# Optimization experiments

Hardware: AMD Instinct MI355X
Metric: run time of the kernel (lower is better)

## Reference

```python
import jax, jax.numpy as jnp
import numpy as np

N_NODES = 100_000
N_EDGES = 3_200_000
HIDDEN = 16


def setup_inputs() -> dict:
    key = jax.random.key(0)
    k1, k2, k3, k4 = jax.random.split(key, 4)
    x = jax.random.normal(k1, (N_NODES, 3), dtype=jnp.float32)
    edge_index = jax.random.randint(k2, (2, N_EDGES), 0, N_NODES, dtype=jnp.int32)
    # Glorot-style init for the two GCN layers (PyG GCNConv: lin weight + bias)
    W1 = jax.random.normal(k3, (3, HIDDEN), dtype=jnp.float32) * (1.0 / np.sqrt(3.0))
    b1 = jnp.zeros((HIDDEN,), dtype=jnp.float32)
    W2 = jax.random.normal(k4, (HIDDEN, 1), dtype=jnp.float32) * (1.0 / np.sqrt(HIDDEN))
    b2 = jnp.zeros((1,), dtype=jnp.float32)
    return {"x": x, "edge_index": edge_index, "W1": W1, "b1": b1, "W2": W2, "b2": b2}


def reference(x, edge_index, W1, b1, W2, b2):
    n = x.shape[0]  # static under jit
    # GCNConv default: add self-loops, symmetric degree normalization
    self_loop = jnp.arange(n, dtype=edge_index.dtype)
    src = jnp.concatenate([edge_index[0], self_loop])
    dst = jnp.concatenate([edge_index[1], self_loop])
    deg = jax.ops.segment_sum(jnp.ones_like(src, dtype=x.dtype), dst, num_segments=n)
    inv_sqrt_deg = jnp.where(deg > 0, jax.lax.rsqrt(jnp.maximum(deg, 1.0)), 0.0)
    norm = inv_sqrt_deg[src] * inv_sqrt_deg[dst]  # [E+N]

    def gcn_conv(h, W, b):
        h = h @ W  # linear transform first (cheaper: small out dim)
        msg = norm[:, None] * h[src]  # gather + scale
        return jax.ops.segment_sum(msg, dst, num_segments=n) + b  # scatter-add

    h = jax.nn.relu(gcn_conv(x, W1, b1))
    out = gcn_conv(h, W2, b2)
    return out.squeeze(-1)  # [N]
```

## Files before the change

kernel.cpp:

```cpp
#include <hip/hip_runtime.h>

#define HIDDEN 16
#define FB 128
#define FB_SHIFT 7
#define NBK_MAX 4096
#define FCHUNK 4096
#define FTH 512
#define STH 512
#define NXCD 8
#define CB 1024
#define CB_SHIFT 10
#define NCB_MAX 512
#define CHUNK 4096
#define SPL 8
#define BT 1024

__device__ __forceinline__ int xcd_chunk(int bid, int nwg) {
    if (nwg < NXCD) return bid;
    int q = nwg / NXCD, r = nwg % NXCD;
    int x = bid % NXCD, k = bid / NXCD;
    return (x < r ? x * (q + 1) : r * (q + 1) + (x - r) * q) + k;
}


__global__ __launch_bounds__(FTH) void
k_histf(const int* __restrict__ dst, int e, int nbk, int nchunk,
        unsigned int* __restrict__ hcT) {
    __shared__ unsigned int h[NBK_MAX];
    for (int i = threadIdx.x; i < nbk; i += FTH) h[i] = 0u;
    __syncthreads();
    int c = xcd_chunk(blockIdx.x, nchunk);
    int start = c * FCHUNK;
    int end = min(start + FCHUNK, e);
    if (end - start == FCHUNK) {
        int i = start + threadIdx.x;
#pragma unroll
        for (int k = 0; k < FCHUNK / FTH; k++, i += FTH)
            atomicAdd(&h[((unsigned)dst[i]) >> FB_SHIFT], 1u);
    } else {
        for (int i = start + threadIdx.x; i < end; i += FTH)
            atomicAdd(&h[((unsigned)dst[i]) >> FB_SHIFT], 1u);
    }
    __syncthreads();
    for (int j = threadIdx.x; j < nbk; j += FTH)
        hcT[(size_t)j * nchunk + c] = h[j];
}

__global__ void k_scanf(unsigned int* __restrict__ hcT,
                        unsigned int* __restrict__ cntc, int nchunk) {
    __shared__ unsigned int ts[256];
    __shared__ unsigned int carry;
    int b = blockIdx.x, t = threadIdx.x;
    if (t == 0) carry = 0u;
    __syncthreads();
    size_t row = (size_t)b * nchunk;
    for (int t0 = 0; t0 < nchunk; t0 += 256) {
        int i = t0 + t;
        unsigned int v = (i < nchunk) ? hcT[row + i] : 0u;
        ts[t] = v;
        __syncthreads();
        for (int off = 1; off < 256; off <<= 1) {
            unsigned int u = (t >= off) ? ts[t - off] : 0u;
            __syncthreads();
            ts[t] += u;
            __syncthreads();
        }
        if (i < nchunk) hcT[row + i] = carry + ts[t] - v;
        __syncthreads();
        if (t == 0) carry += ts[255];
        __syncthreads();
    }
    if (t == 0) cntc[b] = carry;
}

__global__ __launch_bounds__(1024) void
k_scanb(const unsigned int* __restrict__ cntc, int nbk,
        unsigned int* __restrict__ basec,
        unsigned int* __restrict__ rowptr, int n, unsigned int e) {
    __shared__ unsigned int tsum[1024];
    int t = threadIdx.x;
    int K = (nbk + 1023) / 1024;
    unsigned int s = 0;
    for (int k = 0; k < K; k++) {
        int i = t * K + k;
        if (i < nbk) s += cntc[i];
    }
    tsum[t] = s;
    __syncthreads();
    for (int off = 1; off < 1024; off <<= 1) {
        unsigned int v = (t >= off) ? tsum[t - off] : 0u;
        __syncthreads();
        tsum[t] += v;
        __syncthreads();
    }
    unsigned int run = (t == 0) ? 0u : tsum[t - 1];
    for (int k = 0; k < K; k++) {
        int i = t * K + k;
        if (i < nbk) { basec[i] = run; run += cntc[i]; }
    }
    if (t == 1023) basec[nbk] = tsum[1023];
    if (t == 0) rowptr[n] = e;
}

__global__ __launch_bounds__(FTH) void
k_fillf(const int* __restrict__ src, const int* __restrict__ dst,
        int e, int nbk, int nchunk,
        const unsigned int* __restrict__ basec,
        const unsigned int* __restrict__ hcT,
        unsigned int* __restrict__ tmp) {
    __shared__ unsigned int h[NBK_MAX];
    __shared__ unsigned int lb[NBK_MAX];
    int c = xcd_chunk(blockIdx.x, nchunk);
    for (int j = threadIdx.x; j < nbk; j += FTH) {
        lb[j] = basec[j] + hcT[(size_t)j * nchunk + c];
        h[j] = 0u;
    }
    __syncthreads();
    int start = c * FCHUNK;
    int end = min(start + FCHUNK, e);
    if (end - start == FCHUNK) {
        int i = start + threadIdx.x;
#pragma unroll
        for (int k = 0; k < FCHUNK / FTH; k++, i += FTH) {
            unsigned int d = (unsigned)dst[i];
            unsigned int s = (unsigned)src[i];
            unsigned int b = d >> FB_SHIFT;
            unsigned int r = atomicAdd(&h[b], 1u);
            tmp[lb[b] + r] = (s << FB_SHIFT) | (d & (FB - 1u));
        }
    } else {
        for (int i = start + threadIdx.x; i < end; i += FTH) {
            unsigned int d = (unsigned)dst[i];
            unsigned int s = (unsigned)src[i];
            unsigned int b = d >> FB_SHIFT;
            unsigned int r = atomicAdd(&h[b], 1u);
            tmp[lb[b] + r] = (s << FB_SHIFT) | (d & (FB - 1u));
        }
    }
}

__global__ __launch_bounds__(STH) void
k_sortN(const unsigned int* __restrict__ tmp,
        const unsigned int* __restrict__ basec,
        const float* __restrict__ x,
        unsigned int* __restrict__ rowptr, unsigned int* __restrict__ tmp2,
        float4* __restrict__ xs4, int n) {
    __shared__ unsigned int cnt[FB];
    __shared__ unsigned int sc[FB];
    __shared__ unsigned int cur[FB];
    int t = threadIdx.x, b = blockIdx.x;
    unsigned int s = basec[b], endp = basec[b + 1];
    if (t < FB) cnt[t] = 0u;
    __syncthreads();
    for (unsigned int i = s + t; i < endp; i += STH)
        atomicAdd(&cnt[tmp[i] & (FB - 1u)], 1u);
    __syncthreads();
    if (t < FB) sc[t] = cnt[t];
    __syncthreads();
    for (int off = 1; off < FB; off <<= 1) {
        unsigned int v = (t < FB && t >= off) ? sc[t - off] : 0u;
        __syncthreads();
        if (t < FB && t >= off) sc[t] += v;
        __syncthreads();
    }
    if (t < FB) {
        unsigned int excl = sc[t] - cnt[t];
        cur[t] = s + excl;
        int node = (b << FB_SHIFT) + t;
        if (node < n) {
            rowptr[node] = s + excl;
            float iv = rsqrtf((float)(1u + cnt[t]));
            xs4[node] = make_float4(x[3 * node] * iv, x[3 * node + 1] * iv,
                                    x[3 * node + 2] * iv, iv);
        }
    }
    __syncthreads();
    for (unsigned int i = s + t; i < endp; i += STH) {
        unsigned int rec = tmp[i];
        unsigned int r = atomicAdd(&cur[rec & (FB - 1u)], 1u);
        tmp2[r] = rec >> FB_SHIFT;
    }
}

__global__ void k_s1(const unsigned int* __restrict__ rowptr,
                     const unsigned int* __restrict__ tmp2,
                     const float4* __restrict__ xs4,
                     const float* __restrict__ W1, const float* __restrict__ b1,
                     const float* __restrict__ W2, const float* __restrict__ b2,
                     float* __restrict__ t2s, float* __restrict__ out, int n) {
    int gid = blockIdx.x * blockDim.x + threadIdx.x;
    int i = gid >> 1, h = gid & 1;
    bool valid = (i < n);
    unsigned int s = 0, epos = 0;
    if (valid) { s = rowptr[i]; epos = rowptr[i + 1]; }
    unsigned int half = (epos - s) >> 1;
    unsigned int b0 = h ? s + half : s;
    unsigned int b1r = h ? epos : s + half;
    float v0 = 0.f, v1 = 0.f, v2 = 0.f;
    unsigned int j = b0;
    for (; j + 4 <= b1r; j += 4) {
        unsigned a0 = tmp2[j], a1 = tmp2[j + 1], a2 = tmp2[j + 2], a3 = tmp2[j + 3];
        float4 p0 = xs4[a0], p1 = xs4[a1], p2 = xs4[a2], p3 = xs4[a3];
        v0 += (p0.x + p1.x) + (p2.x + p3.x);
        v1 += (p0.y + p1.y) + (p2.y + p3.y);
        v2 += (p0.z + p1.z) + (p2.z + p3.z);
    }
    for (; j < b1r; j++) {
        float4 p = xs4[tmp2[j]];
        v0 += p.x; v1 += p.y; v2 += p.z;
    }
    v0 += __shfl_xor(v0, 1);
    v1 += __shfl_xor(v1, 1);
    v2 += __shfl_xor(v2, 1);
    if (valid && h == 0) {
        float4 me = xs4[i];
        float iv = me.w;
        v0 = (v0 + me.x) * iv;
        v1 = (v1 + me.y) * iv;
        v2 = (v2 + me.z) * iv;
        float acc = 0.f;
#pragma unroll
        for (int k = 0; k < HIDDEN; k++) {
            float hh = fmaxf(fmaf(v0, W1[k], fmaf(v1, W1[HIDDEN + k],
                            fmaf(v2, W1[2 * HIDDEN + k], b1[k]))), 0.f);
            acc += hh * W2[k];
        }
        t2s[i] = acc * iv;
        out[i] = b2[0] + acc * iv * iv;
    }
}

__global__ void k_s2(const unsigned int* __restrict__ rowptr,
                     const unsigned int* __restrict__ tmp2,
                     const float* __restrict__ t2s, const float4* __restrict__ xs4,
                     float* __restrict__ out, int n) {
    int gid = blockIdx.x * blockDim.x + threadIdx.x;
    int i = gid >> 1, h = gid & 1;
    bool valid = (i < n);
    unsigned int s = 0, epos = 0;
    if (valid) { s = rowptr[i]; epos = rowptr[i + 1]; }
    unsigned int half = (epos - s) >> 1;
    unsigned int b0 = h ? s + half : s;
    unsigned int b1r = h ? epos : s + half;
    float v = 0.f;
    unsigned int j = b0;
    for (; j + 4 <= b1r; j += 4) {
        unsigned a0 = tmp2[j], a1 = tmp2[j + 1], a2 = tmp2[j + 2], a3 = tmp2[j + 3];
        v += (t2s[a0] + t2s[a1]) + (t2s[a2] + t2s[a3]);
    }
    for (; j < b1r; j++) v += t2s[tmp2[j]];
    v += __shfl_xor(v, 1);
    if (valid && h == 0) out[i] += v * xs4[i].w;
}


__global__ void k_zero(unsigned int* a, int na) {
    int i = blockIdx.x * blockDim.x + threadIdx.x;
    if (i < na) a[i] = 0u;
}
__global__ void k_hist_c(const int* __restrict__ dst, int e, int ncb, int nchunk,
                         unsigned int* __restrict__ cntc,
                         unsigned int* __restrict__ hcT) {
    __shared__ unsigned int h[NCB_MAX];
    for (int i = threadIdx.x; i < ncb; i += blockDim.x) h[i] = 0u;
    __syncthreads();
    int start = blockIdx.x * CHUNK;
    int end = min(start + CHUNK, e);
    for (int i = start + threadIdx.x; i < end; i += 256)
        atomicAdd(&h[((unsigned)dst[i]) >> CB_SHIFT], 1u);
    __syncthreads();
    for (int j = threadIdx.x; j < ncb; j += blockDim.x) {
        hcT[(size_t)j * nchunk + blockIdx.x] = h[j];
        if (h[j]) atomicAdd(&cntc[j], h[j]);
    }
}
__global__ void k_scan(const unsigned int* __restrict__ cnt, int nb,
                       unsigned int* __restrict__ base) {
    __shared__ unsigned int tsum[256];
    int t = threadIdx.x;
    int K = (nb + 255) / 256;
    unsigned int s = 0;
    for (int k = 0; k < K; k++) {
        int i = t * K + k;
        if (i < nb) s += cnt[i];
    }
    tsum[t] = s;
    __syncthreads();
    for (int off = 1; off < 256; off <<= 1) {
        unsigned int v = (t >= off) ? tsum[t - off] : 0u;
        __syncthreads();
        tsum[t] += v;
        __syncthreads();
    }
    unsigned int run = (t == 0) ? 0u : tsum[t - 1];
    for (int k = 0; k < K; k++) {
        int i = t * K + k;
        if (i < nb) { base[i] = run; run += cnt[i]; }
    }
}
__global__ void k_scanc(const unsigned int* __restrict__ hcT,
                        const unsigned int* __restrict__ basec,
                        unsigned int* __restrict__ lbasec, int nchunk) {
    __shared__ unsigned int ts[256];
    __shared__ unsigned int carry;
    int b = blockIdx.x, t = threadIdx.x;
    if (t == 0) carry = basec[b];
    __syncthreads();
    for (int t0 = 0; t0 < nchunk; t0 += 256) {
        int i = t0 + t;
        unsigned int v = (i < nchunk) ? hcT[(size_t)b * nchunk + i] : 0u;
        ts[t] = v;
        __syncthreads();
        for (int off = 1; off < 256; off <<= 1) {
            unsigned int u = (t >= off) ? ts[t - off] : 0u;
            __syncthreads();
            ts[t] += u;
            __syncthreads();
        }
        if (i < nchunk) lbasec[(size_t)b * nchunk + i] = carry + ts[t] - v;
        __syncthreads();
        if (t == 0) carry += ts[255];
        __syncthreads();
    }
}
__global__ void k_fill_c(const int* __restrict__ src, const int* __restrict__ dst,
                         int e, int ncb, int nchunk,
                         const unsigned int* __restrict__ lbasec,
                         unsigned int* __restrict__ tmp) {
    __shared__ unsigned int h[NCB_MAX];
    __shared__ unsigned int lb[NCB_MAX];
    for (int j = threadIdx.x; j < ncb; j += blockDim.x) {
        lb[j] = lbasec[(size_t)j * nchunk + blockIdx.x];
        h[j] = 0u;
    }
    __syncthreads();
    int start = blockIdx.x * CHUNK;
    int end = min(start + CHUNK, e);
    for (int i = start + threadIdx.x; i < end; i += 256) {
        unsigned int d = (unsigned)dst[i];
        unsigned int b = d >> CB_SHIFT;
        unsigned int r = atomicAdd(&h[b], 1u);
        tmp[lb[b] + r] = (((unsigned)src[i]) << CB_SHIFT) | (d & (CB - 1u));
    }
}
__global__ __launch_bounds__(BT) void
k_deg_split(const unsigned int* __restrict__ tmp, const unsigned int* __restrict__ basec,
            const unsigned int* __restrict__ cntc, unsigned int* __restrict__ deg, int n) {
    __shared__ unsigned int degl[CB];
    int t = threadIdx.x;
    degl[t] = 0u;
    __syncthreads();
    int b = blockIdx.x / SPL, sl = blockIdx.x % SPL;
    unsigned int s = basec[b], m = cntc[b];
    for (unsigned int i = sl * BT + t; i < m; i += SPL * BT)
        atomicAdd(&degl[tmp[s + i] & (CB - 1u)], 1u);
    __syncthreads();
    int node = b * CB + t;
    unsigned int c = degl[t];
    if (node < n && c) atomicAdd(&deg[node], c);
}
__global__ void k_inv_s(const unsigned int* __restrict__ deg, const float* __restrict__ x,
                        float4* __restrict__ xs4, int n) {
    int i = blockIdx.x * blockDim.x + threadIdx.x;
    if (i >= n) return;
    float iv = rsqrtf((float)(deg[i] + 1u));
    xs4[i] = make_float4(x[3 * i] * iv, x[3 * i + 1] * iv, x[3 * i + 2] * iv, iv);
}
__global__ __launch_bounds__(BT) void
k_s1_split(const unsigned int* __restrict__ tmp, const unsigned int* __restrict__ basec,
           const unsigned int* __restrict__ cntc, const float4* __restrict__ xs4,
           float* __restrict__ agg0, float* __restrict__ agg1, float* __restrict__ agg2, int n) {
    __shared__ float a0[CB], a1[CB], a2[CB];
    int t = threadIdx.x;
    a0[t] = 0.f; a1[t] = 0.f; a2[t] = 0.f;
    __syncthreads();
    int b = blockIdx.x / SPL, sl = blockIdx.x % SPL;
    unsigned int s = basec[b], m = cntc[b];
    for (unsigned int i = sl * BT + t; i < m; i += SPL * BT) {
        unsigned rec = tmp[s + i];
        float4 v = xs4[rec >> CB_SHIFT];
        unsigned dl = rec & (CB - 1u);
        atomicAdd(&a0[dl], v.x); atomicAdd(&a1[dl], v.y); atomicAdd(&a2[dl], v.z);
    }
    __syncthreads();
    int node = b * CB + t;
    if (node < n) {
        if (a0[t] != 0.f) atomicAdd(&agg0[node], a0[t]);
        if (a1[t] != 0.f) atomicAdd(&agg1[node], a1[t]);
        if (a2[t] != 0.f) atomicAdd(&agg2[node], a2[t]);
    }
}
__global__ void k_epi_s(const float* __restrict__ agg0, const float* __restrict__ agg1,
                        const float* __restrict__ agg2, const float4* __restrict__ xs4,
                        const float* __restrict__ W1, const float* __restrict__ b1,
                        const float* __restrict__ W2, const float* __restrict__ b2,
                        float* __restrict__ t2s, float* __restrict__ out, int n) {
    int i = blockIdx.x * blockDim.x + threadIdx.x;
    if (i >= n) return;
    float4 xv = xs4[i];
    float iv = xv.w;
    float v0 = iv * (agg0[i] + xv.x), v1 = iv * (agg1[i] + xv.y), v2 = iv * (agg2[i] + xv.z);
    float acc = 0.f;
#pragma unroll
    for (int j = 0; j < HIDDEN; j++) {
        float h = fmaxf(fmaf(v0, W1[j], fmaf(v1, W1[HIDDEN + j],
                       fmaf(v2, W1[2 * HIDDEN + j], b1[j]))), 0.f);
        acc += h * W2[j];
    }
    t2s[i] = acc * iv;
    out[i] = b2[0] + acc * iv * iv;
}
__global__ __launch_bounds__(BT) void
k_s2_split(const unsigned int* __restrict__ tmp, const unsigned int* __restrict__ basec,
           const unsigned int* __restrict__ cntc, const float* __restrict__ t2s,
           const float4* __restrict__ xs4, float* __restrict__ out, int n) {
    __shared__ float o[CB];
    int t = threadIdx.x;
    o[t] = 0.f;
    __syncthreads();
    int b = blockIdx.x / SPL, sl = blockIdx.x % SPL;
    unsigned int s = basec[b], m = cntc[b];
    for (unsigned int i = sl * BT + t; i < m; i += SPL * BT) {
        unsigned rec = tmp[s + i];
        atomicAdd(&o[rec & (CB - 1u)], t2s[rec >> CB_SHIFT]);
    }
    __syncthreads();
    int node = b * CB + t;
    if (node < n && o[t] != 0.f) atomicAdd(&out[node], o[t] * xs4[node].w);
}


extern "C" void kernel_launch(void* const* d_in, const int* in_sizes, int n_in,
                              void* d_out, int out_size, void* d_ws, size_t ws_size,
                              hipStream_t stream) {
    const float* x  = (const float*)d_in[0];
    const int*   ei = (const int*)d_in[1];
    const float* W1 = (const float*)d_in[2];
    const float* b1 = (const float*)d_in[3];
    const float* W2 = (const float*)d_in[4];
    const float* b2 = (const float*)d_in[5];
    float* out = (float*)d_out;

    int n = in_sizes[0] / 3;
    int e = in_sizes[1] / 2;
    const int* src = ei;
    const int* dst = ei + e;
    const int B = 256;

    int nbk = (n + FB - 1) / FB;
    int nchunkf = (e + FCHUNK - 1) / FCHUNK;
    int gridN2 = (2 * n + B - 1) / B;

    size_t needf = (size_t)n * 16 + (size_t)n * 4 + (size_t)(n + 1) * 4
                 + (size_t)(2 * nbk + 1) * 4 + (size_t)nbk * nchunkf * 4
                 + (size_t)e * 8 + 64;

    if (nbk <= NBK_MAX && n < (1 << 25) && ws_size >= needf) {
        float4* xs4 = (float4*)d_ws;
        float* t2s = (float*)(xs4 + n);
        unsigned int* rowptr = (unsigned int*)(t2s + n);
        unsigned int* cntc   = rowptr + (n + 1);
        unsigned int* basec  = cntc + nbk;
        unsigned int* hcT    = basec + nbk + 1;
        unsigned int* tmp    = hcT + (size_t)nbk * nchunkf;
        unsigned int* tmp2   = tmp + e;

        k_histf<<<nchunkf, FTH, 0, stream>>>(dst, e, nbk, nchunkf, hcT);
        k_scanf<<<nbk, 256, 0, stream>>>(hcT, cntc, nchunkf);
        k_scanb<<<1, 1024, 0, stream>>>(cntc, nbk, basec, rowptr, n, (unsigned)e);
        k_fillf<<<nchunkf, FTH, 0, stream>>>(src, dst, e, nbk, nchunkf, basec, hcT, tmp);
        k_sortN<<<nbk, STH, 0, stream>>>(tmp, basec, x, rowptr, tmp2, xs4, n);
        k_s1<<<gridN2, B, 0, stream>>>(rowptr, tmp2, xs4, W1, b1, W2, b2, t2s, out, n);
        k_s2<<<gridN2, B, 0, stream>>>(rowptr, tmp2, t2s, xs4, out, n);
    } else {
        int ncb = (n + CB - 1) / CB;
        int gridE = (e + CHUNK - 1) / CHUNK;
        int gridN = (n + B - 1) / B;
        float4* xs4 = (float4*)d_ws;
        float* agg0 = (float*)(xs4 + n);
        float* agg1 = agg0 + n;
        float* agg2 = agg1 + n;
        unsigned int* deg = (unsigned int*)(agg2 + n);
        float* t2s = (float*)(deg + n);
        unsigned int* cntc   = (unsigned int*)(t2s + n);
        unsigned int* basec  = cntc + ncb;
        unsigned int* hcT    = basec + ncb;
        unsigned int* lbasec = hcT + (size_t)ncb * gridE;
        unsigned int* tmp    = lbasec + (size_t)ncb * gridE;

        k_zero<<<(4 * n + ncb + B - 1) / B, B, 0, stream>>>((unsigned int*)agg0, 4 * n);
        k_zero<<<(ncb + B - 1) / B, B, 0, stream>>>(cntc, ncb);
        k_hist_c<<<gridE, B, 0, stream>>>(dst, e, ncb, gridE, cntc, hcT);
        k_scan<<<1, B, 0, stream>>>(cntc, ncb, basec);
        k_scanc<<<ncb, B, 0, stream>>>(hcT, basec, lbasec, gridE);
        k_fill_c<<<gridE, B, 0, stream>>>(src, dst, e, ncb, gridE, lbasec, tmp);
        k_deg_split<<<ncb * SPL, BT, 0, stream>>>(tmp, basec, cntc, deg, n);
        k_inv_s<<<gridN, B, 0, stream>>>(deg, x, xs4, n);
        k_s1_split<<<ncb * SPL, BT, 0, stream>>>(tmp, basec, cntc, xs4, agg0, agg1, agg2, n);
        k_epi_s<<<gridN, B, 0, stream>>>(agg0, agg1, agg2, xs4, W1, b1, W2, b2, t2s, out, n);
        k_s2_split<<<ncb * SPL, BT, 0, stream>>>(tmp, basec, cntc, t2s, xs4, out, n);
    }
}
```

Before: 181.7 us.

## Replace per-node CSR sort with bucket-level LDS atomic aggregation

Drops the second-level sort that produced a per-node rowptr and sorted source array. Each 128-node bucket block now reads the bucket-sorted packed records directly and accumulates messages with shared-memory float atomics, for both layers. This removes the scatter write to tmp2 and the rowptr array and roughly halves the edge scratch space. In exchange it adds many LDS atomics, up to three per edge in layer one, and makes float summation order nondeterministic.

```diff
diff --git a/kernel.cpp b/kernel.cpp
--- a/kernel.cpp
+++ b/kernel.cpp
@@ -6,7 +6,7 @@
 #define NBK_MAX 4096
 #define FCHUNK 4096
 #define FTH 512
-#define STH 512
+#define ATH 512
 #define NXCD 8
 #define CB 1024
 #define CB_SHIFT 10
@@ -75,8 +75,7 @@
 
 __global__ __launch_bounds__(1024) void
 k_scanb(const unsigned int* __restrict__ cntc, int nbk,
-        unsigned int* __restrict__ basec,
-        unsigned int* __restrict__ rowptr, int n, unsigned int e) {
+        unsigned int* __restrict__ basec) {
     __shared__ unsigned int tsum[1024];
     int t = threadIdx.x;
     int K = (nbk + 1023) / 1024;
@@ -99,7 +98,6 @@
         if (i < nbk) { basec[i] = run; run += cntc[i]; }
     }
     if (t == 1023) basec[nbk] = tsum[1023];
-    if (t == 0) rowptr[n] = e;
 }
 
 __global__ __launch_bounds__(FTH) void
@@ -139,118 +137,120 @@
     }
 }
 
-__global__ __launch_bounds__(STH) void
-k_sortN(const unsigned int* __restrict__ tmp,
-        const unsigned int* __restrict__ basec,
-        const float* __restrict__ x,
-        unsigned int* __restrict__ rowptr, unsigned int* __restrict__ tmp2,
-        float4* __restrict__ xs4, int n) {
+__global__ __launch_bounds__(ATH) void
+k_cnt(const unsigned int* __restrict__ tmp,
+      const unsigned int* __restrict__ basec,
+      const float* __restrict__ x,
+      float4* __restrict__ xs4, int n) {
     __shared__ unsigned int cnt[FB];
-    __shared__ unsigned int sc[FB];
-    __shared__ unsigned int cur[FB];
     int t = threadIdx.x, b = blockIdx.x;
     unsigned int s = basec[b], endp = basec[b + 1];
     if (t < FB) cnt[t] = 0u;
     __syncthreads();
-    for (unsigned int i = s + t; i < endp; i += STH)
+    unsigned int i = s + t;
+    for (; i + 3u * ATH < endp; i += 4u * ATH) {
+        unsigned r0 = tmp[i], r1 = tmp[i + ATH], r2 = tmp[i + 2u * ATH], r3 = tmp[i + 3u * ATH];
+        atomicAdd(&cnt[r0 & (FB - 1u)], 1u);
+        atomicAdd(&cnt[r1 & (FB - 1u)], 1u);
+        atomicAdd(&cnt[r2 & (FB - 1u)], 1u);
+        atomicAdd(&cnt[r3 & (FB - 1u)], 1u);
+    }
+    for (; i < endp; i += ATH)
         atomicAdd(&cnt[tmp[i] & (FB - 1u)], 1u);
     __syncthreads();
-    if (t < FB) sc[t] = cnt[t];
-    __syncthreads();
-    for (int off = 1; off < FB; off <<= 1) {
-        unsigned int v = (t < FB && t >= off) ? sc[t - off] : 0u;
-        __syncthreads();
-        if (t < FB && t >= off) sc[t] += v;
-        __syncthreads();
-    }
     if (t < FB) {
-        unsigned int excl = sc[t] - cnt[t];
-        cur[t] = s + excl;
         int node = (b << FB_SHIFT) + t;
         if (node < n) {
-            rowptr[node] = s + excl;
             float iv = rsqrtf((float)(1u + cnt[t]));
             xs4[node] = make_float4(x[3 * node] * iv, x[3 * node + 1] * iv,
                                     x[3 * node + 2] * iv, iv);
         }
     }
-    __syncthreads();
-    for (unsigned int i = s + t; i < endp; i += STH) {
-        unsigned int rec = tmp[i];
-        unsigned int r = atomicAdd(&cur[rec & (FB - 1u)], 1u);
-        tmp2[r] = rec >> FB_SHIFT;
-    }
-}
-
-__global__ void k_s1(const unsigned int* __restrict__ rowptr,
-                     const unsigned int* __restrict__ tmp2,
-                     const float4* __restrict__ xs4,
-                     const float* __restrict__ W1, const float* __restrict__ b1,
-                     const float* __restrict__ W2, const float* __restrict__ b2,
-                     float* __restrict__ t2s, float* __restrict__ out, int n) {
-    int gid = blockIdx.x * blockDim.x + threadIdx.x;
-    int i = gid >> 1, h = gid & 1;
-    bool valid = (i < n);
-    unsigned int s = 0, epos = 0;
-    if (valid) { s = rowptr[i]; epos = rowptr[i + 1]; }
-    unsigned int half = (epos - s) >> 1;
-    unsigned int b0 = h ? s + half : s;
-    unsigned int b1r = h ? epos : s + half;
-    float v0 = 0.f, v1 = 0.f, v2 = 0.f;
-    unsigned int j = b0;
-    for (; j + 4 <= b1r; j += 4) {
-        unsigned a0 = tmp2[j], a1 = tmp2[j + 1], a2 = tmp2[j + 2], a3 = tmp2[j + 3];
-        float4 p0 = xs4[a0], p1 = xs4[a1], p2 = xs4[a2], p3 = xs4[a3];
-        v0 += (p0.x + p1.x) + (p2.x + p3.x);
-        v1 += (p0.y + p1.y) + (p2.y + p3.y);
-        v2 += (p0.z + p1.z) + (p2.z + p3.z);
-    }
-    for (; j < b1r; j++) {
-        float4 p = xs4[tmp2[j]];
-        v0 += p.x; v1 += p.y; v2 += p.z;
-    }
-    v0 += __shfl_xor(v0, 1);
-    v1 += __shfl_xor(v1, 1);
-    v2 += __shfl_xor(v2, 1);
-    if (valid && h == 0) {
-        float4 me = xs4[i];
-        float iv = me.w;
-        v0 = (v0 + me.x) * iv;
-        v1 = (v1 + me.y) * iv;
-        v2 = (v2 + me.z) * iv;
-        float acc = 0.f;
+}
+
+__global__ __launch_bounds__(ATH) void
+k_s1agg(const unsigned int* __restrict__ tmp,
+        const unsigned int* __restrict__ basec,
+        const float4* __restrict__ xs4,
+        const float* __restrict__ W1, const float* __restrict__ b1,
+        const float* __restrict__ W2, const float* __restrict__ b2,
+        float* __restrict__ t2s, float* __restrict__ out, int n) {
+    __shared__ float a0[FB], a1[FB], a2[FB];
+    int t = threadIdx.x, b = blockIdx.x;
+    unsigned int s = basec[b], endp = basec[b + 1];
+    if (t < FB) { a0[t] = 0.f; a1[t] = 0.f; a2[t] = 0.f; }
+    __syncthreads();
+    unsigned int i = s + t;
+    for (; i + 3u * ATH < endp; i += 4u * ATH) {
+        unsigned r0 = tmp[i], r1 = tmp[i + ATH], r2 = tmp[i + 2u * ATH], r3 = tmp[i + 3u * ATH];
+        float4 p0 = xs4[r0 >> FB_SHIFT];
+        float4 p1 = xs4[r1 >> FB_SHIFT];
+        float4 p2 = xs4[r2 >> FB_SHIFT];
+        float4 p3 = xs4[r3 >> FB_SHIFT];
+        unsigned d0 = r0 & (FB - 1u), d1 = r1 & (FB - 1u);
+        unsigned d2 = r2 & (FB - 1u), d3 = r3 & (FB - 1u);
+        atomicAdd(&a0[d0], p0.x); atomicAdd(&a1[d0], p0.y); atomicAdd(&a2[d0], p0.z);
+        atomicAdd(&a0[d1], p1.x); atomicAdd(&a1[d1], p1.y); atomicAdd(&a2[d1], p1.z);
+        atomicAdd(&a0[d2], p2.x); atomicAdd(&a1[d2], p2.y); atomicAdd(&a2[d2], p2.z);
+        atomicAdd(&a0[d3], p3.x); atomicAdd(&a1[d3], p3.y); atomicAdd(&a2[d3], p3.z);
+    }
+    for (; i < endp; i += ATH) {
+        unsigned rec = tmp[i];
+        float4 p = xs4[rec >> FB_SHIFT];
+        unsigned d = rec & (FB - 1u);
+        atomicAdd(&a0[d], p.x); atomicAdd(&a1[d], p.y); atomicAdd(&a2[d], p.z);
+    }
+    __syncthreads();
+    if (t < FB) {
+        int node = (b << FB_SHIFT) + t;
+        if (node < n) {
+            float4 me = xs4[node];
+            float iv = me.w;
+            float v0 = (a0[t] + me.x) * iv;
+            float v1 = (a1[t] + me.y) * iv;
+            float v2 = (a2[t] + me.z) * iv;
+            float acc = 0.f;
 #pragma unroll
-        for (int k = 0; k < HIDDEN; k++) {
-            float hh = fmaxf(fmaf(v0, W1[k], fmaf(v1, W1[HIDDEN + k],
-                            fmaf(v2, W1[2 * HIDDEN + k], b1[k]))), 0.f);
-            acc += hh * W2[k];
+            for (int k = 0; k < HIDDEN; k++) {
+                float hh = fmaxf(fmaf(v0, W1[k], fmaf(v1, W1[HIDDEN + k],
+                                fmaf(v2, W1[2 * HIDDEN + k], b1[k]))), 0.f);
+                acc += hh * W2[k];
+            }
+            t2s[node] = acc * iv;
+            out[node] = b2[0] + acc * iv * iv;
         }
-        t2s[i] = acc * iv;
-        out[i] = b2[0] + acc * iv * iv;
-    }
-}
-
-__global__ void k_s2(const unsigned int* __restrict__ rowptr,
-                     const unsigned int* __restrict__ tmp2,
-                     const float* __restrict__ t2s, const float4* __restrict__ xs4,
-                     float* __restrict__ out, int n) {
-    int gid = blockIdx.x * blockDim.x + threadIdx.x;
-    int i = gid >> 1, h = gid & 1;
-    bool valid = (i < n);
-    unsigned int s = 0, epos = 0;
-    if (valid) { s = rowptr[i]; epos = rowptr[i + 1]; }
-    unsigned int half = (epos - s) >> 1;
-    unsigned int b0 = h ? s + half : s;
-    unsigned int b1r = h ? epos : s + half;
-    float v = 0.f;
-    unsigned int j = b0;
-    for (; j + 4 <= b1r; j += 4) {
-        unsigned a0 = tmp2[j], a1 = tmp2[j + 1], a2 = tmp2[j + 2], a3 = tmp2[j + 3];
-        v += (t2s[a0] + t2s[a1]) + (t2s[a2] + t2s[a3]);
-    }
-    for (; j < b1r; j++) v += t2s[tmp2[j]];
-    v += __shfl_xor(v, 1);
-    if (valid && h == 0) out[i] += v * xs4[i].w;
+    }
+}
+
+__global__ __launch_bounds__(ATH) void
+k_s2agg(const unsigned int* __restrict__ tmp,
+        const unsigned int* __restrict__ basec,
+        const float* __restrict__ t2s, const float4* __restrict__ xs4,
+        float* __restrict__ out, int n) {
+    __shared__ float o[FB];
+    int t = threadIdx.x, b = blockIdx.x;
+    unsigned int s = basec[b], endp = basec[b + 1];
+    if (t < FB) o[t] = 0.f;
+    __syncthreads();
+    unsigned int i = s + t;
+    for (; i + 3u * ATH < endp; i += 4u * ATH) {
+        unsigned r0 = tmp[i], r1 = tmp[i + ATH], r2 = tmp[i + 2u * ATH], r3 = tmp[i + 3u * ATH];
+        float v0 = t2s[r0 >> FB_SHIFT], v1 = t2s[r1 >> FB_SHIFT];
+        float v2 = t2s[r2 >> FB_SHIFT], v3 = t2s[r3 >> FB_SHIFT];
+        atomicAdd(&o[r0 & (FB - 1u)], v0);
+        atomicAdd(&o[r1 & (FB - 1u)], v1);
+        atomicAdd(&o[r2 & (FB - 1u)], v2);
+        atomicAdd(&o[r3 & (FB - 1u)], v3);
+    }
+    for (; i < endp; i += ATH) {
+        unsigned rec = tmp[i];
+        atomicAdd(&o[rec & (FB - 1u)], t2s[rec >> FB_SHIFT]);
+    }
+    __syncthreads();
+    if (t < FB) {
+        int node = (b << FB_SHIFT) + t;
+        if (node < n) out[node] += o[t] * xs4[node].w;
+    }
 }
 
 
@@ -449,29 +449,26 @@
 
     int nbk = (n + FB - 1) / FB;
     int nchunkf = (e + FCHUNK - 1) / FCHUNK;
-    int gridN2 = (2 * n + B - 1) / B;
-
-    size_t needf = (size_t)n * 16 + (size_t)n * 4 + (size_t)(n + 1) * 4
+
+    size_t needf = (size_t)n * 16 + (size_t)n * 4
                  + (size_t)(2 * nbk + 1) * 4 + (size_t)nbk * nchunkf * 4
-                 + (size_t)e * 8 + 64;
+                 + (size_t)e * 4 + 64;
 
     if (nbk <= NBK_MAX && n < (1 << 25) && ws_size >= needf) {
         float4* xs4 = (float4*)d_ws;
         float* t2s = (float*)(xs4 + n);
-        unsigned int* rowptr = (unsigned int*)(t2s + n);
-        unsigned int* cntc   = rowptr + (n + 1);
+        unsigned int* cntc   = (unsigned int*)(t2s + n);
         unsigned int* basec  = cntc + nbk;
         unsigned int* hcT    = basec + nbk + 1;
         unsigned int* tmp    = hcT + (size_t)nbk * nchunkf;
-        unsigned int* tmp2   = tmp + e;
 
         k_histf<<<nchunkf, FTH, 0, stream>>>(dst, e, nbk, nchunkf, hcT);
         k_scanf<<<nbk, 256, 0, stream>>>(hcT, cntc, nchunkf);
-        k_scanb<<<1, 1024, 0, stream>>>(cntc, nbk, basec, rowptr, n, (unsigned)e);
+        k_scanb<<<1, 1024, 0, stream>>>(cntc, nbk, basec);
         k_fillf<<<nchunkf, FTH, 0, stream>>>(src, dst, e, nbk, nchunkf, basec, hcT, tmp);
-        k_sortN<<<nbk, STH, 0, stream>>>(tmp, basec, x, rowptr, tmp2, xs4, n);
-        k_s1<<<gridN2, B, 0, stream>>>(rowptr, tmp2, xs4, W1, b1, W2, b2, t2s, out, n);
-        k_s2<<<gridN2, B, 0, stream>>>(rowptr, tmp2, t2s, xs4, out, n);
+        k_cnt<<<nbk, ATH, 0, stream>>>(tmp, basec, x, xs4, n);
+        k_s1agg<<<nbk, ATH, 0, stream>>>(tmp, basec, xs4, W1, b1, W2, b2, t2s, out, n);
+        k_s2agg<<<nbk, ATH, 0, stream>>>(tmp, basec, t2s, xs4, out, n);
     } else {
         int ncb = (n + CB - 1) / CB;
         int gridE = (e + CHUNK - 1) / CHUNK;
```

Result: slower. 211.7 us (+16.5%).
